# Performance work log

Measured on AMD Instinct MI355X. Metric: run time of the kernel, lower is better.

## Reference

```python
import jax, jax.numpy as jnp
import numpy as np

H = 768
FF = 3072
NH = 12
DH = H // NH


def setup_inputs() -> dict:
    key = jax.random.key(0)
    ks = jax.random.split(key, 16)
    s = 0.02
    return {
        "latent": jax.random.normal(ks[0], (2, 2048, H), jnp.float32),
        "ln1_w": jnp.ones((H,), jnp.float32),
        "ln1_b": jnp.zeros((H,), jnp.float32),
        "Wq": jax.random.normal(ks[1], (H, H), jnp.float32) * s,
        "bq": jnp.zeros((H,), jnp.float32),
        "Wk": jax.random.normal(ks[2], (H, H), jnp.float32) * s,
        "bk": jnp.zeros((H,), jnp.float32),
        "Wv": jax.random.normal(ks[3], (H, H), jnp.float32) * s,
        "bv": jnp.zeros((H,), jnp.float32),
        "Wo": jax.random.normal(ks[4], (H, H), jnp.float32) * s,
        "bo": jnp.zeros((H,), jnp.float32),
        "ln2_w": jnp.ones((H,), jnp.float32),
        "ln2_b": jnp.zeros((H,), jnp.float32),
        "W1": jax.random.normal(ks[5], (H, FF), jnp.float32) * s,
        "b1": jnp.zeros((FF,), jnp.float32),
        "W2": jax.random.normal(ks[6], (FF, H), jnp.float32) * s,
        "b2": jnp.zeros((H,), jnp.float32),
    }


def _layernorm(x, w, b, eps=1e-6):
    mu = jnp.mean(x, axis=-1, keepdims=True)
    var = jnp.mean(jnp.square(x - mu), axis=-1, keepdims=True)
    return (x - mu) * jax.lax.rsqrt(var + eps) * w + b


def _split_heads(x):  # [B,S,H] -> [B,NH,S,DH]
    B, S, _ = x.shape
    return x.reshape(B, S, NH, DH).transpose(0, 2, 1, 3)


def reference(latent, ln1_w, ln1_b, Wq, bq, Wk, bk, Wv, bv, Wo, bo,
              ln2_w, ln2_b, W1, b1, W2, b2):
    B, S, _ = latent.shape
    # MHSA (dropouts are p=0.0 / eval mode -> identity)
    nx = _layernorm(latent, ln1_w, ln1_b)
    q = _split_heads(nx @ Wq + bq)
    k = _split_heads(nx @ Wk + bk)
    v = _split_heads(nx @ Wv + bv)
    scores = jnp.einsum('bhqd,bhkd->bhqk', q, k) / jnp.sqrt(jnp.float32(DH))
    attn = jax.nn.softmax(scores, axis=-1)
    ctx = jnp.einsum('bhqk,bhkd->bhqd', attn, v)
    ctx = ctx.transpose(0, 2, 1, 3).reshape(B, S, H)
    latent = latent + (ctx @ Wo + bo)
    # FFN (exact erf GELU as in torch nn.GELU default)
    nx = _layernorm(latent, ln2_w, ln2_b)
    h = jax.nn.gelu(nx @ W1 + b1, approximate=False)
    latent = latent + (h @ W2 + b2)
    return latent
```

## Files before the change

### kernel.cpp

```cpp
#include <hip/hip_runtime.h>

#define H 768
#define FF 3072
#define NH 12
#define DH 64
#define SEQ 2048
#define MTOK 4096

typedef __attribute__((ext_vector_type(8))) short short8;
typedef __attribute__((ext_vector_type(4))) float f32x4;
typedef __attribute__((ext_vector_type(2))) unsigned int uint2v;


__device__ __forceinline__ f32x4 mfma16(short8 a, short8 b, f32x4 c) {
  return __builtin_amdgcn_mfma_f32_16x16x32_bf16(a, b, c, 0, 0, 0);
}

__device__ __forceinline__ unsigned short f2bf(float f) {
  union { float f; unsigned int u; } c; c.f = f;
  unsigned int u = c.u;
  u += 0x7fffu + ((u >> 16) & 1u);
  return (unsigned short)(u >> 16);
}
__device__ __forceinline__ float bf2f(unsigned short s) {
  union { unsigned int u; float f; } c; c.u = ((unsigned int)s) << 16;
  return c.f;
}
__device__ __forceinline__ unsigned int pk2bf(float lo, float hi) {
  return (unsigned int)f2bf(lo) | ((unsigned int)f2bf(hi) << 16);
}
__device__ __forceinline__ unsigned int pktrunc(float lo, float hi) {
  union { float f; unsigned int u; } a, b; a.f = hi; b.f = lo;
  return __builtin_amdgcn_perm(a.u, b.u, 0x07060302u);
}

__device__ __forceinline__ void gld16(const unsigned short* g, unsigned short* l) {
  __builtin_amdgcn_global_load_lds(
      (const __attribute__((address_space(1))) void*)g,
      (__attribute__((address_space(3))) void*)l, 16, 0, 0);
}

__global__ __launch_bounds__(256) void prep_kernel(
    const float* __restrict__ Wq, const float* __restrict__ Wk,
    const float* __restrict__ Wv, const float* __restrict__ Wo,
    const float* __restrict__ W1, const float* __restrict__ W2,
    unsigned short* __restrict__ WqkvT, unsigned short* __restrict__ WoT,
    unsigned short* __restrict__ W1T, unsigned short* __restrict__ W2T,
    const float* __restrict__ latent, const float* __restrict__ ln1_w,
    const float* __restrict__ ln1_b, unsigned short* __restrict__ nx) {
  int bid = blockIdx.x;
  int tid = threadIdx.x;
  if (bid >= 6912) {
    int row = bid - 6912;
    const float* xr = latent + (size_t)row * H;
    float v0 = xr[tid], v1 = xr[tid + 256], v2 = xr[tid + 512];
    float s = v0 + v1 + v2;
    float ss = v0 * v0 + v1 * v1 + v2 * v2;
#pragma unroll
    for (int off = 32; off > 0; off >>= 1) {
      s += __shfl_down(s, off);
      ss += __shfl_down(ss, off);
    }
    __shared__ float red[8];
    int wave = tid >> 6, lane = tid & 63;
    if (lane == 0) { red[wave] = s; red[4 + wave] = ss; }
    __syncthreads();
    s = red[0] + red[1] + red[2] + red[3];
    ss = red[4] + red[5] + red[6] + red[7];
    float mu = s * (1.0f / H);
    float var = ss * (1.0f / H) - mu * mu;
    float rs = rsqrtf(var + 1e-6f);
    unsigned short* orow = nx + (size_t)(row >> 4) * (24 * 512) + (row & 15) * 32;
    int col = (tid & 31) ^ ((row & 3) << 3);
    int kb = (tid >> 5) * 512 + col;
    orow[kb]            = f2bf((v0 - mu) * rs * ln1_w[tid]       + ln1_b[tid]);
    orow[kb + 8 * 512]  = f2bf((v1 - mu) * rs * ln1_w[tid + 256] + ln1_b[tid + 256]);
    orow[kb + 16 * 512] = f2bf((v2 - mu) * rs * ln1_w[tid + 512] + ln1_b[tid + 512]);
    return;
  }
  const float* in; unsigned short* out; int K, N, t0;
  if (bid < 1728) {
    K = 768; N = 768;
    if (bid < 576)       { in = Wq; out = WqkvT;                       t0 = bid; }
    else if (bid < 1152) { in = Wk; out = WqkvT + (size_t)768 * 768;   t0 = bid - 576; }
    else                 { in = Wv; out = WqkvT + (size_t)1536 * 768;  t0 = bid - 1152; }
  } else if (bid < 2304) { in = Wo; out = WoT; K = 768;  N = 768;  t0 = bid - 1728; }
  else if (bid < 4608)   { in = W1; out = W1T; K = 768;  N = 3072; t0 = bid - 2304; }
  else                   { in = W2; out = W2T; K = 3072; N = 768;  t0 = bid - 4608; }

  __shared__ float tile[32][33];
  int nb = N >> 5;
  int n0 = (t0 % nb) << 5;
  int k0 = (t0 / nb) << 5;
  int tx = tid & 31, ty = tid >> 5;
#pragma unroll
  for (int yy = 0; yy < 4; ++yy)
    tile[ty + yy * 8][tx] = in[(size_t)(k0 + ty + yy * 8) * N + n0 + tx];
  __syncthreads();
  int KT5 = K >> 5;
#pragma unroll
  for (int yy = 0; yy < 4; ++yy) {
    int n = n0 + ty + yy * 8;
    out[(size_t)((n >> 4) * KT5 + (k0 >> 5)) * 512 + (n & 15) * 32
        + (tx ^ ((n & 3) << 3))]
        = f2bf(tile[tx][ty + yy * 8]);
  }
}

__global__ __launch_bounds__(256) void ln_kernel(const float* __restrict__ x,
                                                 const float* __restrict__ w,
                                                 const float* __restrict__ b,
                                                 unsigned short* __restrict__ out) {
  int row = blockIdx.x;
  int tid = threadIdx.x;
  const float* xr = x + (size_t)row * H;
  float v0 = xr[tid], v1 = xr[tid + 256], v2 = xr[tid + 512];
  float s = v0 + v1 + v2;
  float ss = v0 * v0 + v1 * v1 + v2 * v2;
#pragma unroll
  for (int off = 32; off > 0; off >>= 1) {
    s += __shfl_down(s, off);
    ss += __shfl_down(ss, off);
  }
  __shared__ float red[8];
  int wave = tid >> 6, lane = tid & 63;
  if (lane == 0) { red[wave] = s; red[4 + wave] = ss; }
  __syncthreads();
  s = red[0] + red[1] + red[2] + red[3];
  ss = red[4] + red[5] + red[6] + red[7];
  float mu = s * (1.0f / H);
  float var = ss * (1.0f / H) - mu * mu;
  float rs = rsqrtf(var + 1e-6f);
  unsigned short* orow = out + (size_t)(row >> 4) * (24 * 512) + (row & 15) * 32;
  int col = (tid & 31) ^ ((row & 3) << 3);
  int kb = (tid >> 5) * 512 + col;
  orow[kb]            = f2bf((v0 - mu) * rs * w[tid]       + b[tid]);
  orow[kb + 8 * 512]  = f2bf((v1 - mu) * rs * w[tid + 256] + b[tid + 256]);
  orow[kb + 16 * 512] = f2bf((v2 - mu) * rs * w[tid + 512] + b[tid + 512]);
}

enum { MODE_QKV = 0, MODE_RESID = 1, MODE_GELU = 2 };

template <int MODE>
__global__ __launch_bounds__(256) void gemm128(
    const unsigned short* __restrict__ A,
    const unsigned short* __restrict__ Bt,
    int M, int N, int K,
    const float* __restrict__ bias0,
    const float* __restrict__ bias1,
    const float* __restrict__ bias2,
    unsigned short* __restrict__ out_q,
    unsigned short* __restrict__ out_k,
    unsigned short* __restrict__ out_vT,
    unsigned short* __restrict__ out_bf)
{
  const int mb = M >> 7;
  int m0 = (blockIdx.x % mb) << 7;
  int n0 = (blockIdx.x / mb) << 7;
  int tid = threadIdx.x;
  int wave = tid >> 6, lane = tid & 63;
  int quad = lane >> 4, l16 = lane & 15;
  int wm = (wave & 1) << 6;
  int wn = (wave >> 1) << 6;
  int KT = K >> 5;
  const size_t TS = (size_t)KT * 512;
  int swq = (quad ^ (l16 & 3)) << 3;

  __shared__ __align__(16) unsigned short As[2][128 * 32];
  __shared__ __align__(16) unsigned short Bs[2][128 * 32];

  f32x4 acc[4][4];
#pragma unroll
  for (int i = 0; i < 4; ++i)
#pragma unroll
    for (int j = 0; j < 4; ++j) acc[i][j] = (f32x4){0.f, 0.f, 0.f, 0.f};

  const unsigned short* gA = A + (size_t)((m0 >> 4) + wave * 2) * TS + lane * 8;
  const unsigned short* gB = Bt + (size_t)((n0 >> 4) + wave * 2) * TS + lane * 8;
  unsigned short* lA0 = &As[0][(wave * 32) * 32];
  unsigned short* lA1 = &As[0][(wave * 32 + 16) * 32];
  unsigned short* lB0 = &Bs[0][(wave * 32) * 32];
  unsigned short* lB1 = &Bs[0][(wave * 32 + 16) * 32];
  const int CH = 128 * 32;

  for (int ktb = 0; ktb < KT; ktb += 2) {
#pragma unroll
    for (int kc = 0; kc < 2; ++kc) {
      gld16(gA + (size_t)(ktb + kc) * 512,      lA0 + kc * CH);
      gld16(gA + TS + (size_t)(ktb + kc) * 512, lA1 + kc * CH);
      gld16(gB + (size_t)(ktb + kc) * 512,      lB0 + kc * CH);
      gld16(gB + TS + (size_t)(ktb + kc) * 512, lB1 + kc * CH);
    }
    __syncthreads();
#pragma unroll
    for (int kc = 0; kc < 2; ++kc) {
      short8 af[4], bfr[4];
#pragma unroll
      for (int t = 0; t < 4; ++t)
        af[t] = *(const short8*)(&As[kc][(wm + t * 16 + l16) * 32 + swq]);
#pragma unroll
      for (int t = 0; t < 4; ++t)
        bfr[t] = *(const short8*)(&Bs[kc][(wn + t * 16 + l16) * 32 + swq]);
#pragma unroll
      for (int i = 0; i < 4; ++i)
#pragma unroll
        for (int j = 0; j < 4; ++j)
          acc[i][j] = mfma16(af[i], bfr[j], acc[i][j]);
    }
    __syncthreads();
  }

#pragma unroll
  for (int mt = 0; mt < 4; ++mt)
#pragma unroll
    for (int nt = 0; nt < 4; ++nt) {
      f32x4 c = acc[mt][nt];
      int m = m0 + wm + mt * 16 + quad * 4;
      int n = n0 + wn + nt * 16 + l16;
      if (MODE == MODE_QKV) {
        int bb = m >> 11, sIdx = m & 2047;
        if (n < 768) {
          float bs = bias0[n];
          int hh = n >> 6, d = n & 63;
          unsigned short* dst = out_q + (((size_t)(bb * NH + hh)) * SEQ + sIdx) * DH + d;
#pragma unroll
          for (int r = 0; r < 4; ++r) dst[r * DH] = f2bf(c[r] + bs);
        } else if (n < 1536) {
          int nn = n - 768;
          float bs = bias1[nn];
          int hh = nn >> 6, d = nn & 63;
          size_t base = (size_t)(bb * NH + hh) * (SEQ * DH)
                      + (size_t)(sIdx >> 5) * 2048 + ((sIdx >> 4) & 1) * 1024
                      + (d >> 5) * 512 + (sIdx & 15) * 32 + (d & 31);
#pragma unroll
          for (int r = 0; r < 4; ++r) out_k[base + r * 32] = f2bf(c[r] + bs);
        } else {
          int nn = n - 1536;
          float bs = bias2[nn];
          int hh = nn >> 6, d = nn & 63;
          int k5 = sIdx & 31;
          int sa = (k5 & 0x11) | ((k5 & 0x6) << 1) | ((k5 >> 2) & 0x2);
          size_t cb = (size_t)(bb * NH + hh) * (SEQ * DH)
                    + (size_t)(sIdx >> 5) * 2048 + (d >> 4) * 512
                    + (d & 15) * 8 + (size_t)(sa >> 3) * 128;
          *(unsigned int*)(out_vT + cb + (sa & 7))       = pk2bf(c[0] + bs, c[1] + bs);
          *(unsigned int*)(out_vT + cb + ((sa & 7) | 4)) = pk2bf(c[2] + bs, c[3] + bs);
        }
      } else {
        float bs = bias0[n];
        int mtile = ((m0 + wm) >> 4) + mt;
        unsigned short* opb = out_bf + (size_t)(mtile * (N >> 5) + (n >> 5)) * 512
                              + quad * 4 * 32;
#pragma unroll
        for (int r = 0; r < 4; ++r) {
          float t = c[r] + bs;
          opb[r * 32 + ((n & 31) ^ ((r & 3) << 3))]
              = f2bf(0.5f * t * (1.0f + erff(t * 0.70710678118654752f)));
        }
      }
    }
}

template <int TAG>
__global__ __launch_bounds__(256) void gemm64r(
    const unsigned short* __restrict__ A,
    const unsigned short* __restrict__ Bt,
    int M, int N, int K,
    const float* __restrict__ bias0,
    const float* __restrict__ resid,
    float* __restrict__ out_f)
{
  const int mb = M >> 6;
  int m0 = (blockIdx.x % mb) << 6;
  int n0 = (blockIdx.x / mb) << 6;
  int tid = threadIdx.x;
  int wave = tid >> 6, lane = tid & 63;
  int quad = lane >> 4, l16 = lane & 15;
  int wm = (wave & 1) << 5;
  int wn = (wave >> 1) << 5;
  int KT = K >> 5;
  const size_t TS = (size_t)KT * 512;
  int swq = (quad ^ (l16 & 3)) << 3;

  __shared__ __align__(16) unsigned short As[4][64 * 32];
  __shared__ __align__(16) unsigned short Bs[4][64 * 32];

  f32x4 acc[2][2];
#pragma unroll
  for (int i = 0; i < 2; ++i)
#pragma unroll
    for (int j = 0; j < 2; ++j) acc[i][j] = (f32x4){0.f, 0.f, 0.f, 0.f};

  const unsigned short* gA = A + (size_t)((m0 >> 4) + wave) * TS + lane * 8;
  const unsigned short* gB = Bt + (size_t)((n0 >> 4) + wave) * TS + lane * 8;
  unsigned short* lA = &As[0][wave * 512];
  unsigned short* lB = &Bs[0][wave * 512];
  const int CH = 64 * 32;

  for (int ktb = 0; ktb < KT; ktb += 4) {
#pragma unroll
    for (int kc = 0; kc < 4; ++kc) {
      gld16(gA + (size_t)(ktb + kc) * 512, lA + kc * CH);
      gld16(gB + (size_t)(ktb + kc) * 512, lB + kc * CH);
    }
    __syncthreads();
#pragma unroll
    for (int kc = 0; kc < 4; ++kc) {
      short8 af[2], bfr[2];
#pragma unroll
      for (int t = 0; t < 2; ++t)
        af[t] = *(const short8*)(&As[kc][(wm + t * 16 + l16) * 32 + swq]);
#pragma unroll
      for (int t = 0; t < 2; ++t)
        bfr[t] = *(const short8*)(&Bs[kc][(wn + t * 16 + l16) * 32 + swq]);
#pragma unroll
      for (int i = 0; i < 2; ++i)
#pragma unroll
        for (int j = 0; j < 2; ++j)
          acc[i][j] = mfma16(af[i], bfr[j], acc[i][j]);
    }
    __syncthreads();
  }

#pragma unroll
  for (int mt = 0; mt < 2; ++mt)
#pragma unroll
    for (int nt = 0; nt < 2; ++nt) {
      f32x4 c = acc[mt][nt];
      int m = m0 + wm + mt * 16 + quad * 4;
      int n = n0 + wn + nt * 16 + l16;
      float bs = bias0[n];
      const float* rp = resid + (size_t)m * N + n;
      float* op = out_f + (size_t)m * N + n;
#pragma unroll
      for (int r = 0; r < 4; ++r) op[(size_t)r * N] = rp[(size_t)r * N] + c[r] + bs;
    }
}

__global__ __launch_bounds__(256, 4) void flash_attn_kernel(
    const unsigned short* __restrict__ q,
    const unsigned short* __restrict__ k,
    const unsigned short* __restrict__ vT,
    unsigned short* __restrict__ ctx)
{
  const float CEXP = 0.18033688011112042f;
  int bh = blockIdx.x % 24;
  int qblk = blockIdx.x / 24;
  int b = bh / NH, h = bh % NH;
  int tid = threadIdx.x;
  int wave = tid >> 6, lane = tid & 63;
  int quad = lane >> 4, l16 = lane & 15;
  int qbase = qblk << 5;

  const unsigned short* qp = q + ((size_t)bh * SEQ + qbase) * DH;
  const unsigned short* kbh = k + (size_t)bh * (SEQ * DH);
  const unsigned short* vbh = vT + (size_t)bh * (SEQ * DH);

  short8 qf00 = *(const short8*)(qp + l16 * DH + quad * 8);
  short8 qf01 = *(const short8*)(qp + l16 * DH + 32 + quad * 8);
  short8 qf10 = *(const short8*)(qp + (16 + l16) * DH + quad * 8);
  short8 qf11 = *(const short8*)(qp + (16 + l16) * DH + 32 + quad * 8);

  f32x4 oacc[2][4];
#pragma unroll
  for (int t = 0; t < 2; ++t)
#pragma unroll
    for (int dt = 0; dt < 4; ++dt) oacc[t][dt] = (f32x4){0.f, 0.f, 0.f, 0.f};
  float L[2] = {0.f, 0.f};

  int klin = (l16 * 4 + quad) * 8;
  int vlin = (quad * 16 + l16) * 8;

  int keylo = wave << 9;
  for (int key0 = keylo; key0 < keylo + 512; key0 += 32) {
    int cbase = (key0 >> 5) * 2048;
    short8 ka0 = *(const short8*)(kbh + cbase + klin);
    short8 ka1 = *(const short8*)(kbh + cbase + 512 + klin);
    short8 kb0 = *(const short8*)(kbh + cbase + 1024 + klin);
    short8 kb1 = *(const short8*)(kbh + cbase + 1536 + klin);
    short8 vf0 = *(const short8*)(vbh + cbase + 0 * 512 + vlin);
    short8 vf1 = *(const short8*)(vbh + cbase + 1 * 512 + vlin);
    short8 vf2 = *(const short8*)(vbh + cbase + 2 * 512 + vlin);
    short8 vf3 = *(const short8*)(vbh + cbase + 3 * 512 + vlin);

#pragma unroll
    for (int t = 0; t < 2; ++t) {
      short8 q0 = t ? qf10 : qf00;
      short8 q1 = t ? qf11 : qf01;
      f32x4 s0 = (f32x4){0.f, 0.f, 0.f, 0.f};
      f32x4 s1 = (f32x4){0.f, 0.f, 0.f, 0.f};
      s0 = mfma16(ka0, q0, s0);
      s0 = mfma16(ka1, q1, s0);
      s1 = mfma16(kb0, q0, s1);
      s1 = mfma16(kb1, q1, s1);

      f32x4 p0, p1;
#pragma unroll
      for (int r = 0; r < 4; ++r) {
        p0[r] = __builtin_amdgcn_exp2f(s0[r] * CEXP);
        p1[r] = __builtin_amdgcn_exp2f(s1[r] * CEXP);
      }
      L[t] += (p0[0] + p0[1]) + (p0[2] + p0[3]) + (p1[0] + p1[1]) + (p1[2] + p1[3]);

      unsigned int d00 = pktrunc(p0[0], p0[1]);
      unsigned int d01 = pktrunc(p0[2], p0[3]);
      unsigned int d10 = pktrunc(p1[0], p1[1]);
      unsigned int d11 = pktrunc(p1[2], p1[3]);

      uint2v rA = __builtin_amdgcn_permlane32_swap(d00, d10, false, false);
      uint2v rB = __builtin_amdgcn_permlane32_swap(d01, d11, false, false);
      union { short8 s; unsigned int i[4]; } pf;
      pf.i[0] = rA[0];
      pf.i[1] = rA[1];
      pf.i[2] = rB[0];
      pf.i[3] = rB[1];

      oacc[t][0] = mfma16(vf0, pf.s, oacc[t][0]);
      oacc[t][1] = mfma16(vf1, pf.s, oacc[t][1]);
      oacc[t][2] = mfma16(vf2, pf.s, oacc[t][2]);
      oacc[t][3] = mfma16(vf3, pf.s, oacc[t][3]);
    }
  }

#pragma unroll
  for (int t = 0; t < 2; ++t) {
    L[t] += __shfl_xor(L[t], 16);
    L[t] += __shfl_xor(L[t], 32);
  }

  __shared__ float lbuf[4][2][16];
  __shared__ uint2 obuf[4][2][4][64];

  if (lane < 16) {
    lbuf[wave][0][lane] = L[0];
    lbuf[wave][1][lane] = L[1];
  }
#pragma unroll
  for (int t = 0; t < 2; ++t)
#pragma unroll
    for (int dt = 0; dt < 4; ++dt) {
      uint2 pk;
      pk.x = pk2bf(oacc[t][dt][0], oacc[t][dt][1]);
      pk.y = pk2bf(oacc[t][dt][2], oacc[t][dt][3]);
      obuf[wave][t][dt][lane] = pk;
    }
  __syncthreads();

#pragma unroll
  for (int pp = 0; pp < 2; ++pp) {
    int pi = wave * 2 + pp;
    int t = pi >> 2, dt = pi & 3;
    f32x4 sum = (f32x4){0.f, 0.f, 0.f, 0.f};
#pragma unroll
    for (int w = 0; w < 4; ++w) {
      uint2 pk = obuf[w][t][dt][lane];
      sum[0] += bf2f((unsigned short)(pk.x & 0xffff));
      sum[1] += bf2f((unsigned short)(pk.x >> 16));
      sum[2] += bf2f((unsigned short)(pk.y & 0xffff));
      sum[3] += bf2f((unsigned short)(pk.y >> 16));
    }
    float lstar = lbuf[0][t][l16] + lbuf[1][t][l16] + lbuf[2][t][l16] + lbuf[3][t][l16];
    float rinv = 1.0f / lstar;
    uint2 res;
    res.x = pk2bf(sum[0] * rinv, sum[1] * rinv);
    res.y = pk2bf(sum[2] * rinv, sum[3] * rinv);
    int colsw = (((dt & 1) * 16 + quad * 4)) ^ ((l16 & 3) << 3);
    unsigned short* crow = ctx
        + ((size_t)((b * SEQ + qbase + t * 16) >> 4) * 24 + h * 2 + (dt >> 1)) * 512
        + l16 * 32 + colsw;
    *(uint2*)crow = res;
  }
}

extern "C" void kernel_launch(void* const* d_in, const int* in_sizes, int n_in,
                              void* d_out, int out_size, void* d_ws, size_t ws_size,
                              hipStream_t stream) {
  const float* latent = (const float*)d_in[0];
  const float* ln1_w = (const float*)d_in[1];
  const float* ln1_b = (const float*)d_in[2];
  const float* Wq = (const float*)d_in[3];
  const float* bq = (const float*)d_in[4];
  const float* Wk = (const float*)d_in[5];
  const float* bk = (const float*)d_in[6];
  const float* Wv = (const float*)d_in[7];
  const float* bv = (const float*)d_in[8];
  const float* Wo = (const float*)d_in[9];
  const float* bo = (const float*)d_in[10];
  const float* ln2_w = (const float*)d_in[11];
  const float* ln2_b = (const float*)d_in[12];
  const float* W1 = (const float*)d_in[13];
  const float* b1 = (const float*)d_in[14];
  const float* W2 = (const float*)d_in[15];
  const float* b2 = (const float*)d_in[16];
  float* out = (float*)d_out;

  char* ws = (char*)d_ws;
  unsigned short* WqkvT = (unsigned short*)ws; ws += (size_t)2304 * 768 * 2;
  unsigned short* WoT   = (unsigned short*)ws; ws += (size_t)768 * 768 * 2;
  unsigned short* W1T   = (unsigned short*)ws; ws += (size_t)3072 * 768 * 2;
  unsigned short* W2T   = (unsigned short*)ws; ws += (size_t)768 * 3072 * 2;
  unsigned short* nx    = (unsigned short*)ws; ws += (size_t)MTOK * H * 2;
  unsigned short* nx2   = (unsigned short*)ws; ws += (size_t)MTOK * H * 2;
  unsigned short* qb    = (unsigned short*)ws; ws += (size_t)MTOK * H * 2;
  unsigned short* kb    = (unsigned short*)ws; ws += (size_t)MTOK * H * 2;
  unsigned short* vTb   = (unsigned short*)ws; ws += (size_t)MTOK * H * 2;
  unsigned short* ctx   = (unsigned short*)ws; ws += (size_t)MTOK * H * 2;
  unsigned short* hbuf  = (unsigned short*)ws; ws += (size_t)MTOK * FF * 2;
  float* x1             = (float*)ws;          ws += (size_t)MTOK * H * 4;

  prep_kernel<<<6912 + MTOK, 256, 0, stream>>>(
      Wq, Wk, Wv, Wo, W1, W2, WqkvT, WoT, W1T, W2T,
      latent, ln1_w, ln1_b, nx);

  gemm128<MODE_QKV><<<32 * 18, 256, 0, stream>>>(
      nx, WqkvT, MTOK, 2304, 768, bq, bk, bv,
      qb, kb, vTb, nullptr);

  flash_attn_kernel<<<24 * 64, 256, 0, stream>>>(qb, kb, vTb, ctx);

  gemm64r<0><<<64 * 12, 256, 0, stream>>>(
      ctx, WoT, MTOK, 768, 768, bo, latent, x1);

  ln_kernel<<<MTOK, 256, 0, stream>>>(x1, ln2_w, ln2_b, nx2);

  gemm128<MODE_GELU><<<32 * 24, 256, 0, stream>>>(
      nx2, W1T, MTOK, 3072, 768, b1, nullptr, nullptr,
      nullptr, nullptr, nullptr, hbuf);

  gemm64r<1><<<64 * 12, 256, 0, stream>>>(
      hbuf, W2T, MTOK, 768, 3072, b2, x1, out);
}
```

Baseline: 258.9 us.

## Replace 4-wave 128x128 GEMM with single-wave 64x64 double-buffered pipelined GEMM

The QKV and FFN1 GEMMs now run as one-wave blocks, each computing a 64x64 tile, instead of four-wave blocks computing 128x128 tiles. The K loop becomes a software pipeline: the next K slice is prefetched into the other LDS buffer while the current one is computed, using explicit vmcnt and lgkmcnt waits in place of __syncthreads. This is meant to remove block-level barrier stalls and to raise the number of blocks and their occupancy. In exchange, each block loads twice as much global data per FLOP, and the extra MFMA interleaving across waves now depends on the scheduler.

```diff
diff --git a/kernel.cpp b/kernel.cpp
--- a/kernel.cpp
+++ b/kernel.cpp
@@ -142,7 +142,7 @@
 enum { MODE_QKV = 0, MODE_RESID = 1, MODE_GELU = 2 };
 
 template <int MODE>
-__global__ __launch_bounds__(256) void gemm128(
+__global__ __launch_bounds__(64, 4) void gemm1w(
     const unsigned short* __restrict__ A,
     const unsigned short* __restrict__ Bt,
     int M, int N, int K,
@@ -154,20 +154,17 @@
     unsigned short* __restrict__ out_vT,
     unsigned short* __restrict__ out_bf)
 {
-  const int mb = M >> 7;
-  int m0 = (blockIdx.x % mb) << 7;
-  int n0 = (blockIdx.x / mb) << 7;
-  int tid = threadIdx.x;
-  int wave = tid >> 6, lane = tid & 63;
+  const int mb = M >> 6;
+  int m0 = (blockIdx.x % mb) << 6;
+  int n0 = (blockIdx.x / mb) << 6;
+  int lane = threadIdx.x;
   int quad = lane >> 4, l16 = lane & 15;
-  int wm = (wave & 1) << 6;
-  int wn = (wave >> 1) << 6;
   int KT = K >> 5;
   const size_t TS = (size_t)KT * 512;
   int swq = (quad ^ (l16 & 3)) << 3;
 
-  __shared__ __align__(16) unsigned short As[2][128 * 32];
-  __shared__ __align__(16) unsigned short Bs[2][128 * 32];
+  __shared__ __align__(16) unsigned short As[2][4][512];
+  __shared__ __align__(16) unsigned short Bs[2][4][512];
 
   f32x4 acc[4][4];
 #pragma unroll
@@ -175,48 +172,49 @@
 #pragma unroll
     for (int j = 0; j < 4; ++j) acc[i][j] = (f32x4){0.f, 0.f, 0.f, 0.f};
 
-  const unsigned short* gA = A + (size_t)((m0 >> 4) + wave * 2) * TS + lane * 8;
-  const unsigned short* gB = Bt + (size_t)((n0 >> 4) + wave * 2) * TS + lane * 8;
-  unsigned short* lA0 = &As[0][(wave * 32) * 32];
-  unsigned short* lA1 = &As[0][(wave * 32 + 16) * 32];
-  unsigned short* lB0 = &Bs[0][(wave * 32) * 32];
-  unsigned short* lB1 = &Bs[0][(wave * 32 + 16) * 32];
-  const int CH = 128 * 32;
-
-  for (int ktb = 0; ktb < KT; ktb += 2) {
-#pragma unroll
-    for (int kc = 0; kc < 2; ++kc) {
-      gld16(gA + (size_t)(ktb + kc) * 512,      lA0 + kc * CH);
-      gld16(gA + TS + (size_t)(ktb + kc) * 512, lA1 + kc * CH);
-      gld16(gB + (size_t)(ktb + kc) * 512,      lB0 + kc * CH);
-      gld16(gB + TS + (size_t)(ktb + kc) * 512, lB1 + kc * CH);
-    }
-    __syncthreads();
-#pragma unroll
-    for (int kc = 0; kc < 2; ++kc) {
-      short8 af[4], bfr[4];
-#pragma unroll
-      for (int t = 0; t < 4; ++t)
-        af[t] = *(const short8*)(&As[kc][(wm + t * 16 + l16) * 32 + swq]);
-#pragma unroll
-      for (int t = 0; t < 4; ++t)
-        bfr[t] = *(const short8*)(&Bs[kc][(wn + t * 16 + l16) * 32 + swq]);
-#pragma unroll
-      for (int i = 0; i < 4; ++i)
-#pragma unroll
-        for (int j = 0; j < 4; ++j)
-          acc[i][j] = mfma16(af[i], bfr[j], acc[i][j]);
-    }
-    __syncthreads();
-  }
+  const unsigned short* gA = A + (size_t)(m0 >> 4) * TS + lane * 8;
+  const unsigned short* gB = Bt + (size_t)(n0 >> 4) * TS + lane * 8;
+
+#define STAGE1(b, kt) do { \
+    _Pragma("unroll") \
+    for (int t = 0; t < 4; ++t) gld16(gA + (size_t)t * TS + (size_t)(kt) * 512, &As[b][t][0]); \
+    _Pragma("unroll") \
+    for (int t = 0; t < 4; ++t) gld16(gB + (size_t)t * TS + (size_t)(kt) * 512, &Bs[b][t][0]); \
+  } while (0)
+
+#define COMPUTE1(b) do { \
+    short8 af[4], bfr[4]; \
+    _Pragma("unroll") \
+    for (int t = 0; t < 4; ++t) af[t] = *(const short8*)(&As[b][t][l16 * 32 + swq]); \
+    _Pragma("unroll") \
+    for (int t = 0; t < 4; ++t) bfr[t] = *(const short8*)(&Bs[b][t][l16 * 32 + swq]); \
+    _Pragma("unroll") \
+    for (int i = 0; i < 4; ++i) \
+      _Pragma("unroll") \
+      for (int j = 0; j < 4; ++j) \
+        acc[i][j] = mfma16(af[i], bfr[j], acc[i][j]); \
+  } while (0)
+
+  STAGE1(0, 0);
+  for (int it = 0; it < KT; ++it) {
+    int ktn = (it + 1 < KT) ? it + 1 : 0;
+    STAGE1((it + 1) & 1, ktn);
+    asm volatile("s_waitcnt vmcnt(8)" ::: "memory");
+    __builtin_amdgcn_sched_barrier(0);
+    COMPUTE1(it & 1);
+    asm volatile("s_waitcnt lgkmcnt(0)" ::: "memory");
+    __builtin_amdgcn_sched_barrier(0);
+  }
+#undef STAGE1
+#undef COMPUTE1
 
 #pragma unroll
   for (int mt = 0; mt < 4; ++mt)
 #pragma unroll
     for (int nt = 0; nt < 4; ++nt) {
       f32x4 c = acc[mt][nt];
-      int m = m0 + wm + mt * 16 + quad * 4;
-      int n = n0 + wn + nt * 16 + l16;
+      int m = m0 + mt * 16 + quad * 4;
+      int n = n0 + nt * 16 + l16;
       if (MODE == MODE_QKV) {
         int bb = m >> 11, sIdx = m & 2047;
         if (n < 768) {
@@ -248,7 +246,7 @@
         }
       } else {
         float bs = bias0[n];
-        int mtile = ((m0 + wm) >> 4) + mt;
+        int mtile = (m0 >> 4) + mt;
         unsigned short* opb = out_bf + (size_t)(mtile * (N >> 5) + (n >> 5)) * 512
                               + quad * 4 * 32;
 #pragma unroll
@@ -512,7 +510,7 @@
       Wq, Wk, Wv, Wo, W1, W2, WqkvT, WoT, W1T, W2T,
       latent, ln1_w, ln1_b, nx);
 
-  gemm128<MODE_QKV><<<32 * 18, 256, 0, stream>>>(
+  gemm1w<MODE_QKV><<<64 * 36, 64, 0, stream>>>(
       nx, WqkvT, MTOK, 2304, 768, bq, bk, bv,
       qb, kb, vTb, nullptr);
 
@@ -523,7 +521,7 @@
 
   ln_kernel<<<MTOK, 256, 0, stream>>>(x1, ln2_w, ln2_b, nx2);
 
-  gemm128<MODE_GELU><<<32 * 24, 256, 0, stream>>>(
+  gemm1w<MODE_GELU><<<64 * 48, 64, 0, stream>>>(
       nx2, W1T, MTOK, 3072, 768, b1, nullptr, nullptr,
       nullptr, nullptr, nullptr, hbuf);
 
```

Result: slower. 271.1 us (+4.7%).
